# Kernel optimization log

Measured on AMD Instinct MI355X. Metric: run time of the kernel, lower is better.

Reference implementation:

```python
import jax, jax.numpy as jnp
import numpy as np

B, N, L, K = 32, 512, 8, 8


def setup_inputs() -> dict:
    key = jax.random.key(0)
    k1, k2 = jax.random.split(key)
    A = jax.random.normal(k1, (B, N, N), dtype=jnp.float32)
    A = 0.5 * (A + A.transpose(0, 2, 1))  # symmetric matrix, as in MMF use-case
    O_stack = jax.random.normal(k2, (L, B, K, K), dtype=jnp.float32)  # per-level KxK rotations
    rng = np.random.default_rng(0)
    idx = np.stack([np.sort(rng.choice(N, K, replace=False)) for _ in range(B * L)])
    indices = jnp.asarray(idx.reshape(B, L, K), dtype=jnp.int32)  # sorted, distinct per (b,l)
    wavelet = indices[:, :, 0]  # wavelet index is one of the selected indices per level
    return {"A": A, "O_stack": O_stack, "indices": indices, "wavelet": wavelet}


def reference(A, O_stack, indices, wavelet):
    Bz, Nz, _ = A.shape
    Lz = O_stack.shape[0]
    eye = jnp.eye(Nz, dtype=A.dtype)

    def build_U(idx, O):
        # identity except the KxK block at (idx_i, idx_j) replaced by O
        # (matches torch boolean-mask row-major fill since idx is sorted)
        return eye.at[idx[:, None], idx[None, :]].set(O)

    right = None
    for l in range(Lz):
        U = jax.vmap(build_U)(indices[:, l], O_stack[l])  # [B,N,N]
        right = U if l == 0 else U @ right
        A = U @ A @ U.transpose(0, 2, 1)

    # final masking: zero rows/cols of wavelet indices, keep diagonal
    active = jnp.ones((Bz, Nz), dtype=A.dtype).at[jnp.arange(Bz)[:, None], wavelet].set(0.0)
    left = active[:, :, None] * active[:, None, :]
    d = jnp.arange(Nz)
    left = left.at[:, d, d].set(1.0)
    D = A * left
    A_rec = right.transpose(0, 2, 1) @ D @ right
    return (A_rec, right, D)
```

## Files before the change

kernel.cpp:

```cpp
#include <hip/hip_runtime.h>

#define BATCH 32
#define NDIM 512
#define LNUM 8
#define KDIM 8

#define WS_PM     0
#define WS_ACT    640
#define WS_RAT    78976
#define WS_RDT    111744
#define WS_STRIDE 144512

#define LSTR 65
typedef float f4 __attribute__((ext_vector_type(4)));

__global__ __launch_bounds__(256) void k_prep(
    const float* __restrict__ A, const float* __restrict__ O,
    const int* __restrict__ indices, const int* __restrict__ wavelet,
    float* __restrict__ ws, float* __restrict__ out)
{
    const int b  = blockIdx.x;
    const int cy = blockIdx.y;
    const int tid = threadIdx.x;
    float* base = ws + (size_t)b * WS_STRIDE;
    const size_t seg = (size_t)BATCH*NDIM*NDIM;

    __shared__ float Wl[64*LSTR];
    __shared__ __align__(16) float Buf1[64*LSTR];
    __shared__ __align__(16) float Buf2[64*LSTR];
    __shared__ __align__(16) float Buf3[64*LSTR];
    __shared__ int   pml[NDIM];
    __shared__ float actl[NDIM];
    __shared__ float actS[64];
    __shared__ int   idxsh[64];
    __shared__ int   Ssh[64];
    __shared__ float Oall[LNUM*KDIM*KDIM];
    __shared__ int   s_sh;

    for (int t = tid; t < LNUM*KDIM*KDIM; t += 256) {
        int l = t >> 6, k = t & 63;
        Oall[t] = O[((size_t)l*BATCH + b)*(KDIM*KDIM) + k];
    }
    if (tid < 64) idxsh[tid] = indices[b*64 + tid];
    for (int n = tid; n < NDIM; n += 256) { pml[n] = -1; actl[n] = 1.f; }
    __syncthreads();

    const int wv = tid >> 6;
    const int ln = tid & 63;
    int s_reg = 0;

    if (wv == 0) {
        int n = idxsh[ln];
        bool first = true;
        for (int t = 0; t < ln; ++t) if (idxsh[t] == n) first = false;
        unsigned long long m = __ballot(first);
        int rank = __popcll(m & ((1ull << ln) - 1ull));
        s_reg = (int)__popcll(m);
        if (first) { pml[n] = rank; Ssh[rank] = n; }
        if (ln >= s_reg) Ssh[ln] = 0;
        if (ln < LNUM) actl[wavelet[b*LNUM + ln]] = 0.f;
        if (ln == 0) s_sh = s_reg;
    }
    __syncthreads();

    if (wv == 0) {
        actS[ln] = actl[Ssh[ln]];
        for (int rr = 0; rr < 64; ++rr)
            Wl[rr*LSTR + ln] = (rr == ln && rr < s_reg) ? 1.f : 0.f;
        for (int l = 0; l < LNUM; ++l) {
            int pr[KDIM];
            float wcol[KDIM], accv[KDIM];
            #pragma unroll
            for (int j = 0; j < KDIM; ++j) pr[j] = pml[idxsh[l*KDIM + j]];
            #pragma unroll
            for (int j = 0; j < KDIM; ++j) wcol[j] = Wl[pr[j]*LSTR + ln];
            #pragma unroll
            for (int i = 0; i < KDIM; ++i) {
                float a = 0.f;
                #pragma unroll
                for (int j = 0; j < KDIM; ++j)
                    a += Oall[l*64 + i*KDIM + j] * wcol[j];
                accv[i] = a;
            }
            #pragma unroll
            for (int i = 0; i < KDIM; ++i) Wl[pr[i]*LSTR + ln] = accv[i];
        }
    } else {
        if (cy < 8) {
            const int j0 = cy * 64;
            for (int t = tid - 64; t < 1024; t += 192) {
                int n = t >> 4, cc = t & 15;
                f4 v = ((const f4*)(A + ((size_t)b*NDIM + Ssh[n])*NDIM + j0))[cc];
                ((f4*)(Buf1 + n*64))[cc] = v;
            }
        } else {
            for (int t = tid - 64; t < 4096; t += 192) {
                int n = t >> 6, mm = t & 63;
                Buf1[n*LSTR + mm] = A[((size_t)b*NDIM + Ssh[n])*NDIM + Ssh[mm]];
            }
            int*   g_posmap = (int*)(base + WS_PM);
            float* g_act    = base + WS_ACT;
            for (int n = tid - 64; n < NDIM; n += 192) {
                g_posmap[n] = pml[n]; g_act[n] = actl[n];
            }
        }
    }
    __syncthreads();
    const int s = s_sh;

    if (cy < 8) {
        const int j0 = cy * 64;
        float* AS  = Buf1;
        float* RAt = Buf2;
        float* g_RAT = base + WS_RAT;
        float* g_RDT = base + WS_RDT;

        const int g = wv;
        const int j = ln;
        const int jg = j0 + j;
        const int pj = pml[jg];
        const float aj = actl[jg];
        float racc[16];

        #pragma unroll
        for (int k = 0; k < 16; ++k) racc[k] = 0.f;
        for (int n = 0; n < 64; ++n) {
            float av = AS[n*64 + j];
            #pragma unroll
            for (int k = 0; k < 16; ++k) racc[k] += Wl[(g*16 + k)*LSTR + n] * av;
        }
        #pragma unroll
        for (int k = 0; k < 16; ++k) RAt[(g*16 + k)*64 + j] = racc[k];
        {
            f4* dst = (f4*)(g_RAT + (size_t)jg*64 + g*16);
            #pragma unroll
            for (int q = 0; q < 4; ++q) {
                f4 v = { racc[4*q], racc[4*q+1], racc[4*q+2], racc[4*q+3] };
                dst[q] = v;
            }
        }
        if (pj < 0) {
            #pragma unroll
            for (int k = 0; k < 16; ++k) {
                int r = g*16 + k;
                if (r < s) {
                    size_t ro = ((size_t)b*NDIM + Ssh[r])*NDIM + jg;
                    out[2*seg + ro] = racc[k] * actS[r] * aj;
                    out[seg + ro]   = 0.f;
                }
            }
        }
        __syncthreads();

        #pragma unroll
        for (int k = 0; k < 16; ++k) racc[k] = 0.f;
        for (int n = 0; n < 64; ++n) {
            float dt = actS[n] * RAt[n*64 + j];
            #pragma unroll
            for (int k = 0; k < 16; ++k) racc[k] += Wl[n*LSTR + g*16 + k] * dt;
        }
        #pragma unroll
        for (int k = 0; k < 16; ++k) racc[k] *= aj;
        {
            f4* dst = (f4*)(g_RDT + (size_t)jg*64 + g*16);
            #pragma unroll
            for (int q = 0; q < 4; ++q) {
                f4 v = { racc[4*q], racc[4*q+1], racc[4*q+2], racc[4*q+3] };
                dst[q] = v;
            }
        }
        if (pj < 0) {
            #pragma unroll
            for (int k = 0; k < 16; ++k) {
                int r = g*16 + k;
                if (r < s) {
                    size_t ro = ((size_t)b*NDIM + Ssh[r])*NDIM + jg;
                    out[ro] = racc[k];
                }
            }
        }
    } else {
        const int w = wv;
        float acc[16];

        #pragma unroll
        for (int k = 0; k < 16; ++k) acc[k] = 0.f;
        for (int n = 0; n < 64; ++n) {
            float as = Buf1[n*LSTR + ln];
            #pragma unroll
            for (int k = 0; k < 16; ++k) acc[k] += Wl[(w*16 + k)*LSTR + n] * as;
        }
        #pragma unroll
        for (int k = 0; k < 16; ++k) Buf2[(w*16 + k)*LSTR + ln] = acc[k];
        __syncthreads();

        #pragma unroll
        for (int k = 0; k < 16; ++k) acc[k] = 0.f;
        for (int m = 0; m < 64; ++m) {
            float wvv = Wl[ln*LSTR + m];
            #pragma unroll
            for (int k = 0; k < 16; ++k) acc[k] += Buf2[(w*16 + k)*LSTR + m] * wvv;
        }
        #pragma unroll
        for (int k = 0; k < 16; ++k) Buf3[(w*16 + k)*LSTR + ln] = acc[k];
        __syncthreads();

        for (int t = tid; t < 4096; t += 256) {
            int n = t >> 6, m = t & 63;
            float mv = (Ssh[n] == Ssh[m]) ? 1.f : actS[n]*actS[m];
            Buf1[n*LSTR + m] = mv * Buf3[n*LSTR + m];
        }
        __syncthreads();

        #pragma unroll
        for (int k = 0; k < 16; ++k) acc[k] = 0.f;
        for (int n = 0; n < 64; ++n) {
            float dv = Buf1[n*LSTR + ln];
            #pragma unroll
            for (int k = 0; k < 16; ++k) acc[k] += Wl[n*LSTR + (w*16 + k)] * dv;
        }
        #pragma unroll
        for (int k = 0; k < 16; ++k) Buf2[(w*16 + k)*LSTR + ln] = acc[k];
        __syncthreads();

        #pragma unroll
        for (int k = 0; k < 16; ++k) acc[k] = 0.f;
        for (int m = 0; m < 64; ++m) {
            float wvv = Wl[m*LSTR + ln];
            #pragma unroll
            for (int k = 0; k < 16; ++k) acc[k] += Buf2[(w*16 + k)*LSTR + m] * wvv;
        }
        if (ln < s) {
            #pragma unroll
            for (int k = 0; k < 16; ++k) {
                int p = w*16 + k;
                if (p < s) {
                    size_t ro = ((size_t)b*NDIM + Ssh[p])*NDIM + Ssh[ln];
                    out[ro]         = acc[k];
                    out[seg + ro]   = Wl[p*LSTR + ln];
                    out[2*seg + ro] = Buf1[p*LSTR + ln];
                }
            }
        }
    }
}

__global__ __launch_bounds__(256) void k_big(const float* __restrict__ A,
                                             const float* __restrict__ ws,
                                             float* __restrict__ out)
{
    const int b = blockIdx.y;
    const int rh = threadIdx.x >> 7;
    const int lane = threadIdx.x & 127;
    const int i = blockIdx.x*2 + rh;
    const int j0 = lane*4;

    const float* base = ws + (size_t)b * WS_STRIDE;
    const int*   posmap = (const int*)(base + WS_PM);
    const float* act = base + WS_ACT;
    const float* RAT = base + WS_RAT;
    const float* RDT = base + WS_RDT;

    const int pi = posmap[i];
    if (pi >= 0) return;

    const float acti = act[i];
    const size_t rowoff = ((size_t)b*NDIM + i)*NDIM;
    const size_t seg = (size_t)BATCH*NDIM*NDIM;

    int4   p4  = ((const int4*)posmap)[lane];
    float4 aj4 = ((const float4*)act)[lane];
    int   pm[4] = {p4.x, p4.y, p4.z, p4.w};
    float aj[4] = {aj4.x, aj4.y, aj4.z, aj4.w};

    const float* rat = RAT + (size_t)i*64;
    const float* rdt = RDT + (size_t)i*64;

    float a[4], arec[4], dv[4], rv[4];
    f4 v = __builtin_nontemporal_load((const f4*)(A + rowoff) + lane);
    a[0]=v.x; a[1]=v.y; a[2]=v.z; a[3]=v.w;
    #pragma unroll
    for (int c = 0; c < 4; ++c) {
        int pj = pm[c];
        if (pj >= 0) a[c] = rat[pj];
        float mv = (i == j0 + c) ? 1.f : acti * aj[c];
        dv[c] = a[c] * mv;
        arec[c] = (pj < 0) ? dv[c] : rdt[pj];
        rv[c] = (i == j0 + c) ? 1.f : 0.f;
    }

    f4 o0; o0.x = arec[0]; o0.y = arec[1]; o0.z = arec[2]; o0.w = arec[3];
    f4 o1; o1.x = rv[0];   o1.y = rv[1];   o1.z = rv[2];   o1.w = rv[3];
    f4 o2; o2.x = dv[0];   o2.y = dv[1];   o2.z = dv[2];   o2.w = dv[3];
    __builtin_nontemporal_store(o0, (f4*)(out + rowoff) + lane);
    __builtin_nontemporal_store(o1, (f4*)(out + seg + rowoff) + lane);
    __builtin_nontemporal_store(o2, (f4*)(out + 2*seg + rowoff) + lane);
}

extern "C" void kernel_launch(void* const* d_in, const int* in_sizes, int n_in,
                              void* d_out, int out_size, void* d_ws, size_t ws_size,
                              hipStream_t stream) {
    const float* A       = (const float*)d_in[0];
    const float* O       = (const float*)d_in[1];
    const int*   indices = (const int*)d_in[2];
    const int*   wavelet = (const int*)d_in[3];
    float* ws  = (float*)d_ws;
    float* out = (float*)d_out;

    k_prep<<<dim3(BATCH, 9), 256, 0, stream>>>(A, O, indices, wavelet, ws, out);
    k_big <<<dim3(NDIM/2, BATCH), 256, 0, stream>>>(A, ws, out);
}
```

Before: 178.9 us.

## Fuse prep and streaming kernels into one launch, recomputing small projections per block

```diff
diff --git a/kernel.cpp b/kernel.cpp
--- a/kernel.cpp
+++ b/kernel.cpp
@@ -4,39 +4,50 @@
 #define NDIM 512
 #define LNUM 8
 #define KDIM 8
-
-#define WS_PM     0
-#define WS_ACT    640
-#define WS_RAT    78976
-#define WS_RDT    111744
-#define WS_STRIDE 144512
-
 #define LSTR 65
+#define ROWS 8
+#define NPREP (BATCH*9)
+#define NBIG  (BATCH*(NDIM/ROWS))
+
 typedef float f4 __attribute__((ext_vector_type(4)));
 
-__global__ __launch_bounds__(256) void k_prep(
+__global__ __launch_bounds__(256, 4) void k_all(
     const float* __restrict__ A, const float* __restrict__ O,
     const int* __restrict__ indices, const int* __restrict__ wavelet,
-    float* __restrict__ ws, float* __restrict__ out)
+    float* __restrict__ out)
 {
-    const int b  = blockIdx.x;
-    const int cy = blockIdx.y;
+    const int id  = blockIdx.x;
     const int tid = threadIdx.x;
-    float* base = ws + (size_t)b * WS_STRIDE;
+    const int wv  = tid >> 6;
+    const int ln  = tid & 63;
+    const bool prep = (id < NPREP);
+    int b, cy, xg;
+    if (prep) { b = id / 9; cy = id % 9; xg = 0; }
+    else      { int t = id - NPREP; b = t & 31; xg = t >> 5; cy = -1; }
     const size_t seg = (size_t)BATCH*NDIM*NDIM;
 
     __shared__ float Wl[64*LSTR];
-    __shared__ __align__(16) float Buf1[64*LSTR];
-    __shared__ __align__(16) float Buf2[64*LSTR];
-    __shared__ __align__(16) float Buf3[64*LSTR];
-    __shared__ int   pml[NDIM];
-    __shared__ float actl[NDIM];
+    __shared__ __align__(16) float BufA[64*64];
+    __shared__ __align__(16) int   pml[NDIM];
+    __shared__ __align__(16) float actl[NDIM];
     __shared__ float actS[64];
     __shared__ int   idxsh[64];
     __shared__ int   Ssh[64];
     __shared__ float Oall[LNUM*KDIM*KDIM];
     __shared__ int   s_sh;
 
+    f4 ar0a, ar0b, ar1a, ar1b;
+    int i0 = 0;
+    if (!prep) {
+        i0 = xg*ROWS + 2*wv;
+        const float* r0 = A + ((size_t)b*NDIM + i0)*NDIM;
+        const float* r1 = r0 + NDIM;
+        ar0a = __builtin_nontemporal_load((const f4*)r0 + ln);
+        ar0b = __builtin_nontemporal_load((const f4*)r0 + 64 + ln);
+        ar1a = __builtin_nontemporal_load((const f4*)r1 + ln);
+        ar1b = __builtin_nontemporal_load((const f4*)r1 + 64 + ln);
+    }
+
     for (int t = tid; t < LNUM*KDIM*KDIM; t += 256) {
         int l = t >> 6, k = t & 63;
         Oall[t] = O[((size_t)l*BATCH + b)*(KDIM*KDIM) + k];
@@ -45,10 +56,7 @@
     for (int n = tid; n < NDIM; n += 256) { pml[n] = -1; actl[n] = 1.f; }
     __syncthreads();
 
-    const int wv = tid >> 6;
-    const int ln = tid & 63;
     int s_reg = 0;
-
     if (wv == 0) {
         int n = idxsh[ln];
         bool first = true;
@@ -68,8 +76,7 @@
         for (int rr = 0; rr < 64; ++rr)
             Wl[rr*LSTR + ln] = (rr == ln && rr < s_reg) ? 1.f : 0.f;
         for (int l = 0; l < LNUM; ++l) {
-            int pr[KDIM];
-            float wcol[KDIM], accv[KDIM];
+            int pr[KDIM]; float wcol[KDIM], accv[KDIM];
             #pragma unroll
             for (int j = 0; j < KDIM; ++j) pr[j] = pml[idxsh[l*KDIM + j]];
             #pragma unroll
@@ -86,38 +93,33 @@
             for (int i = 0; i < KDIM; ++i) Wl[pr[i]*LSTR + ln] = accv[i];
         }
     } else {
-        if (cy < 8) {
-            const int j0 = cy * 64;
-            for (int t = tid - 64; t < 1024; t += 192) {
-                int n = t >> 4, cc = t & 15;
-                f4 v = ((const f4*)(A + ((size_t)b*NDIM + Ssh[n])*NDIM + j0))[cc];
-                ((f4*)(Buf1 + n*64))[cc] = v;
+        if (prep) {
+            if (cy < 8) {
+                const int j0 = cy * 64;
+                for (int t = tid - 64; t < 1024; t += 192) {
+                    int n = t >> 4, cc = t & 15;
+                    f4 v = ((const f4*)(A + ((size_t)b*NDIM + Ssh[n])*NDIM + j0))[cc];
+                    ((f4*)(BufA + n*64))[cc] = v;
+                }
+            } else {
+                for (int t = tid - 64; t < 4096; t += 192) {
+                    int n = t >> 6, mm = t & 63;
+                    BufA[n*64 + mm] = A[((size_t)b*NDIM + Ssh[n])*NDIM + Ssh[mm]];
+                }
             }
         } else {
-            for (int t = tid - 64; t < 4096; t += 192) {
-                int n = t >> 6, mm = t & 63;
-                Buf1[n*LSTR + mm] = A[((size_t)b*NDIM + Ssh[n])*NDIM + Ssh[mm]];
-            }
-            int*   g_posmap = (int*)(base + WS_PM);
-            float* g_act    = base + WS_ACT;
-            for (int n = tid - 64; n < NDIM; n += 192) {
-                g_posmap[n] = pml[n]; g_act[n] = actl[n];
+            for (int t = tid - 64; t < ROWS*64; t += 192) {
+                int r = t >> 6, n = t & 63;
+                BufA[t] = A[((size_t)b*NDIM + xg*ROWS + r)*NDIM + Ssh[n]];
             }
         }
     }
     __syncthreads();
     const int s = s_sh;
 
-    if (cy < 8) {
-        const int j0 = cy * 64;
-        float* AS  = Buf1;
-        float* RAt = Buf2;
-        float* g_RAT = base + WS_RAT;
-        float* g_RDT = base + WS_RDT;
-
-        const int g = wv;
-        const int j = ln;
-        const int jg = j0 + j;
+    if (prep && cy < 8) {
+        const int g = wv, j = ln;
+        const int jg = cy*64 + j;
         const int pj = pml[jg];
         const float aj = actl[jg];
         float racc[16];
@@ -125,19 +127,9 @@
         #pragma unroll
         for (int k = 0; k < 16; ++k) racc[k] = 0.f;
         for (int n = 0; n < 64; ++n) {
-            float av = AS[n*64 + j];
+            float av = BufA[n*64 + j];
             #pragma unroll
             for (int k = 0; k < 16; ++k) racc[k] += Wl[(g*16 + k)*LSTR + n] * av;
-        }
-        #pragma unroll
-        for (int k = 0; k < 16; ++k) RAt[(g*16 + k)*64 + j] = racc[k];
-        {
-            f4* dst = (f4*)(g_RAT + (size_t)jg*64 + g*16);
-            #pragma unroll
-            for (int q = 0; q < 4; ++q) {
-                f4 v = { racc[4*q], racc[4*q+1], racc[4*q+2], racc[4*q+3] };
-                dst[q] = v;
-            }
         }
         if (pj < 0) {
             #pragma unroll
@@ -151,23 +143,16 @@
             }
         }
         __syncthreads();
+        #pragma unroll
+        for (int k = 0; k < 16; ++k) BufA[(g*16 + k)*64 + j] = racc[k];
+        __syncthreads();
 
         #pragma unroll
         for (int k = 0; k < 16; ++k) racc[k] = 0.f;
         for (int n = 0; n < 64; ++n) {
-            float dt = actS[n] * RAt[n*64 + j];
+            float dt = actS[n] * BufA[n*64 + j];
             #pragma unroll
             for (int k = 0; k < 16; ++k) racc[k] += Wl[n*LSTR + g*16 + k] * dt;
-        }
-        #pragma unroll
-        for (int k = 0; k < 16; ++k) racc[k] *= aj;
-        {
-            f4* dst = (f4*)(g_RDT + (size_t)jg*64 + g*16);
-            #pragma unroll
-            for (int q = 0; q < 4; ++q) {
-                f4 v = { racc[4*q], racc[4*q+1], racc[4*q+2], racc[4*q+3] };
-                dst[q] = v;
-            }
         }
         if (pj < 0) {
             #pragma unroll
@@ -175,23 +160,24 @@
                 int r = g*16 + k;
                 if (r < s) {
                     size_t ro = ((size_t)b*NDIM + Ssh[r])*NDIM + jg;
-                    out[ro] = racc[k];
-                }
-            }
-        }
-    } else {
+                    out[ro] = racc[k] * aj;
+                }
+            }
+        }
+    } else if (prep) {
         const int w = wv;
         float acc[16];
 
         #pragma unroll
         for (int k = 0; k < 16; ++k) acc[k] = 0.f;
         for (int n = 0; n < 64; ++n) {
-            float as = Buf1[n*LSTR + ln];
+            float as = BufA[n*64 + ln];
             #pragma unroll
             for (int k = 0; k < 16; ++k) acc[k] += Wl[(w*16 + k)*LSTR + n] * as;
         }
-        #pragma unroll
-        for (int k = 0; k < 16; ++k) Buf2[(w*16 + k)*LSTR + ln] = acc[k];
+        __syncthreads();
+        #pragma unroll
+        for (int k = 0; k < 16; ++k) BufA[(w*16 + k)*64 + ln] = acc[k];
         __syncthreads();
 
         #pragma unroll
@@ -199,36 +185,26 @@
         for (int m = 0; m < 64; ++m) {
             float wvv = Wl[ln*LSTR + m];
             #pragma unroll
-            for (int k = 0; k < 16; ++k) acc[k] += Buf2[(w*16 + k)*LSTR + m] * wvv;
-        }
-        #pragma unroll
-        for (int k = 0; k < 16; ++k) Buf3[(w*16 + k)*LSTR + ln] = acc[k];
+            for (int k = 0; k < 16; ++k) acc[k] += BufA[(w*16 + k)*64 + m] * wvv;
+        }
+        __syncthreads();
+        #pragma unroll
+        for (int k = 0; k < 16; ++k) BufA[(w*16 + k)*64 + ln] = acc[k];
         __syncthreads();
 
         for (int t = tid; t < 4096; t += 256) {
             int n = t >> 6, m = t & 63;
             float mv = (Ssh[n] == Ssh[m]) ? 1.f : actS[n]*actS[m];
-            Buf1[n*LSTR + m] = mv * Buf3[n*LSTR + m];
+            BufA[t] *= mv;
         }
         __syncthreads();
 
         #pragma unroll
         for (int k = 0; k < 16; ++k) acc[k] = 0.f;
         for (int n = 0; n < 64; ++n) {
-            float dv = Buf1[n*LSTR + ln];
-            #pragma unroll
-            for (int k = 0; k < 16; ++k) acc[k] += Wl[n*LSTR + (w*16 + k)] * dv;
-        }
-        #pragma unroll
-        for (int k = 0; k < 16; ++k) Buf2[(w*16 + k)*LSTR + ln] = acc[k];
-        __syncthreads();
-
-        #pragma unroll
-        for (int k = 0; k < 16; ++k) acc[k] = 0.f;
-        for (int m = 0; m < 64; ++m) {
-            float wvv = Wl[m*LSTR + ln];
-            #pragma unroll
-            for (int k = 0; k < 16; ++k) acc[k] += Buf2[(w*16 + k)*LSTR + m] * wvv;
+            float dvv = BufA[n*64 + ln];
+            #pragma unroll
+            for (int k = 0; k < 16; ++k) acc[k] += Wl[n*LSTR + (w*16 + k)] * dvv;
         }
         if (ln < s) {
             #pragma unroll
@@ -236,65 +212,96 @@
                 int p = w*16 + k;
                 if (p < s) {
                     size_t ro = ((size_t)b*NDIM + Ssh[p])*NDIM + Ssh[ln];
-                    out[ro]         = acc[k];
                     out[seg + ro]   = Wl[p*LSTR + ln];
-                    out[2*seg + ro] = Buf1[p*LSTR + ln];
-                }
-            }
-        }
-    }
-}
-
-__global__ __launch_bounds__(256) void k_big(const float* __restrict__ A,
-                                             const float* __restrict__ ws,
-                                             float* __restrict__ out)
-{
-    const int b = blockIdx.y;
-    const int rh = threadIdx.x >> 7;
-    const int lane = threadIdx.x & 127;
-    const int i = blockIdx.x*2 + rh;
-    const int j0 = lane*4;
-
-    const float* base = ws + (size_t)b * WS_STRIDE;
-    const int*   posmap = (const int*)(base + WS_PM);
-    const float* act = base + WS_ACT;
-    const float* RAT = base + WS_RAT;
-    const float* RDT = base + WS_RDT;
-
-    const int pi = posmap[i];
-    if (pi >= 0) return;
-
-    const float acti = act[i];
-    const size_t rowoff = ((size_t)b*NDIM + i)*NDIM;
-    const size_t seg = (size_t)BATCH*NDIM*NDIM;
-
-    int4   p4  = ((const int4*)posmap)[lane];
-    float4 aj4 = ((const float4*)act)[lane];
-    int   pm[4] = {p4.x, p4.y, p4.z, p4.w};
-    float aj[4] = {aj4.x, aj4.y, aj4.z, aj4.w};
-
-    const float* rat = RAT + (size_t)i*64;
-    const float* rdt = RDT + (size_t)i*64;
-
-    float a[4], arec[4], dv[4], rv[4];
-    f4 v = __builtin_nontemporal_load((const f4*)(A + rowoff) + lane);
-    a[0]=v.x; a[1]=v.y; a[2]=v.z; a[3]=v.w;
-    #pragma unroll
-    for (int c = 0; c < 4; ++c) {
-        int pj = pm[c];
-        if (pj >= 0) a[c] = rat[pj];
-        float mv = (i == j0 + c) ? 1.f : acti * aj[c];
-        dv[c] = a[c] * mv;
-        arec[c] = (pj < 0) ? dv[c] : rdt[pj];
-        rv[c] = (i == j0 + c) ? 1.f : 0.f;
-    }
-
-    f4 o0; o0.x = arec[0]; o0.y = arec[1]; o0.z = arec[2]; o0.w = arec[3];
-    f4 o1; o1.x = rv[0];   o1.y = rv[1];   o1.z = rv[2];   o1.w = rv[3];
-    f4 o2; o2.x = dv[0];   o2.y = dv[1];   o2.z = dv[2];   o2.w = dv[3];
-    __builtin_nontemporal_store(o0, (f4*)(out + rowoff) + lane);
-    __builtin_nontemporal_store(o1, (f4*)(out + seg + rowoff) + lane);
-    __builtin_nontemporal_store(o2, (f4*)(out + 2*seg + rowoff) + lane);
+                    out[2*seg + ro] = BufA[p*64 + ln];
+                }
+            }
+        }
+        __syncthreads();
+        #pragma unroll
+        for (int k = 0; k < 16; ++k) BufA[(w*16 + k)*64 + ln] = acc[k];
+        __syncthreads();
+
+        #pragma unroll
+        for (int k = 0; k < 16; ++k) acc[k] = 0.f;
+        for (int m = 0; m < 64; ++m) {
+            float wvv = Wl[m*LSTR + ln];
+            #pragma unroll
+            for (int k = 0; k < 16; ++k) acc[k] += BufA[(w*16 + k)*64 + m] * wvv;
+        }
+        if (ln < s) {
+            #pragma unroll
+            for (int k = 0; k < 16; ++k) {
+                int p = w*16 + k;
+                if (p < s) {
+                    size_t ro = ((size_t)b*NDIM + Ssh[p])*NDIM + Ssh[ln];
+                    out[ro] = acc[k];
+                }
+            }
+        }
+    } else {
+        float* aSl  = BufA;
+        float* ratl = BufA + 512;
+        float* rdtl = BufA + 1024;
+
+        #pragma unroll
+        for (int rr = 0; rr < 2; ++rr) {
+            const int r = 2*wv + rr;
+            float acc = 0.f;
+            for (int n = 0; n < 64; ++n)
+                acc += Wl[ln*LSTR + n] * aSl[r*64 + n];
+            ratl[r*64 + ln] = acc;
+        }
+        __syncthreads();
+
+        #pragma unroll
+        for (int rr = 0; rr < 2; ++rr) {
+            const int r = 2*wv + rr;
+            float acc = 0.f;
+            for (int n = 0; n < 64; ++n)
+                acc += Wl[n*LSTR + ln] * (actS[n] * ratl[r*64 + n]);
+            rdtl[r*64 + ln] = acc * actl[i0 + rr];
+        }
+        __syncthreads();
+
+        #pragma unroll
+        for (int rr = 0; rr < 2; ++rr) {
+            const int i = i0 + rr;
+            if (pml[i] >= 0) continue;
+            const float acti = actl[i];
+            const float* ratr = ratl + (2*wv + rr)*64;
+            const float* rdtr = rdtl + (2*wv + rr)*64;
+            const size_t rowoff = ((size_t)b*NDIM + i)*NDIM;
+            #pragma unroll
+            for (int h = 0; h < 2; ++h) {
+                const int l4 = ln + 64*h;
+                const int jb = l4*4;
+                f4 av = (rr == 0) ? (h == 0 ? ar0a : ar0b)
+                                  : (h == 0 ? ar1a : ar1b);
+                int4 p4 = ((const int4*)pml)[l4];
+                f4   a4 = ((const f4*)actl)[l4];
+                int   pm[4] = {p4.x, p4.y, p4.z, p4.w};
+                float aj[4] = {a4.x, a4.y, a4.z, a4.w};
+                float a[4]  = {av.x, av.y, av.z, av.w};
+                float arec[4], dv[4], rv[4];
+                #pragma unroll
+                for (int c = 0; c < 4; ++c) {
+                    int pj = pm[c];
+                    if (pj >= 0) a[c] = ratr[pj];
+                    float mv = (i == jb + c) ? 1.f : acti * aj[c];
+                    dv[c] = a[c] * mv;
+                    arec[c] = (pj < 0) ? dv[c] : rdtr[pj];
+                    rv[c] = (i == jb + c) ? 1.f : 0.f;
+                }
+                f4 o0 = {arec[0], arec[1], arec[2], arec[3]};
+                f4 o1 = {rv[0],   rv[1],   rv[2],   rv[3]};
+                f4 o2 = {dv[0],   dv[1],   dv[2],   dv[3]};
+                __builtin_nontemporal_store(o0, (f4*)(out + rowoff) + l4);
+                __builtin_nontemporal_store(o1, (f4*)(out + seg + rowoff) + l4);
+                __builtin_nontemporal_store(o2, (f4*)(out + 2*seg + rowoff) + l4);
+            }
+        }
+    }
 }
 
 extern "C" void kernel_launch(void* const* d_in, const int* in_sizes, int n_in,
@@ -304,9 +311,8 @@
     const float* O       = (const float*)d_in[1];
     const int*   indices = (const int*)d_in[2];
     const int*   wavelet = (const int*)d_in[3];
-    float* ws  = (float*)d_ws;
     float* out = (float*)d_out;
-
-    k_prep<<<dim3(BATCH, 9), 256, 0, stream>>>(A, O, indices, wavelet, ws, out);
-    k_big <<<dim3(NDIM/2, BATCH), 256, 0, stream>>>(A, ws, out);
+    (void)d_ws; (void)ws_size;
+
+    k_all<<<dim3(NPREP + NBIG), 256, 0, stream>>>(A, O, indices, wavelet, out);
 }
```

Result: slower. 194.9 us (+9.0%).
